# Kernel optimization log

Measured on AMD Instinct MI355X. Metric: run time of the kernel, lower is better.

Reference implementation:

```python
import jax, jax.numpy as jnp
import numpy as np

OUT, IN, GS = 8192, 8192, 128
N_GROUPS = OUT * IN // GS  # 524288


def setup_inputs() -> dict:
    key = jax.random.key(0)
    k1, k2, k3 = jax.random.split(key, 3)
    x = jax.random.normal(k1, (32, IN), dtype=jnp.float32)
    # ternary values in {-1, 0, 1}
    ternary = jax.random.randint(k2, (OUT, IN), -1, 2, dtype=jnp.int32)
    # positive per-group scales
    scales = jax.random.uniform(k3, (N_GROUPS,), dtype=jnp.float32, minval=0.01, maxval=0.1)
    return {"x": x, "ternary": ternary, "scales": scales}


def reference(x, ternary, scales):
    # Dequantize: each contiguous group of GS weights shares one scale.
    # scales: [n_groups] -> [n_groups, GS] -> [OUT, IN]
    scales_exp = jnp.broadcast_to(scales[:, None], (N_GROUPS, GS)).reshape(OUT, IN)
    w = ternary.astype(jnp.float32) * scales_exp  # [OUT, IN]
    # F.linear(x, w) = x @ w.T
    return jnp.einsum("ti,oi->to", x, w)
```

## Files before the change

kernel.cpp:

```cpp
#include <hip/hip_runtime.h>
#include <stdint.h>

#define OUT_DIM 8192
#define IN_DIM  8192
#define GS      128
#define MROWS   32
#define NSPLIT  8
#define KCHUNK  1024
#define KS      64
#define NSTG    (KCHUNK / KS)
#define PART_ELEMS (MROWS * OUT_DIM)

typedef __attribute__((ext_vector_type(8))) short bf16x8;
typedef __attribute__((ext_vector_type(4))) float f32x4;
typedef __attribute__((ext_vector_type(8))) unsigned short u16x8;
typedef __attribute__((ext_vector_type(2))) unsigned short u16x2;
typedef __attribute__((ext_vector_type(4))) unsigned int   u32x4;

__device__ __forceinline__ unsigned short f2bf_rne(float f) {
    uint32_t v = __builtin_bit_cast(uint32_t, f);
    v += 0x7FFFu + ((v >> 16) & 1u);
    return (unsigned short)(v >> 16);
}

__global__ __launch_bounds__(256) void prep_xbf(const float* __restrict__ x,
                                                unsigned short* __restrict__ xbf) {
    int i = (blockIdx.x * 256 + threadIdx.x) * 8;
    float4 a = *(const float4*)(x + i);
    float4 b = *(const float4*)(x + i + 4);
    float f[8] = {a.x, a.y, a.z, a.w, b.x, b.y, b.z, b.w};
    u16x8 u;
#pragma unroll
    for (int j = 0; j < 8; ++j) u[j] = f2bf_rne(f[j]);
    *(u16x8*)(xbf + i) = u;
}

__device__ __forceinline__ unsigned int cvt2(int t0, int t1, unsigned int p32) {
    unsigned int t16 = __builtin_amdgcn_perm((unsigned int)t1, (unsigned int)t0,
                                             0x05040100u);
    unsigned int v   = p32 | (t16 & 0x80008000u);
    u16x2 r = __builtin_bit_cast(u16x2, v) *
              __builtin_bit_cast(u16x2, t16 & 0x00010001u);
    return __builtin_bit_cast(unsigned int, r);
}

__device__ __forceinline__ bf16x8 conv8(const int4 wa, const int4 wb, unsigned int p32) {
    u32x4 d;
    d[0] = cvt2(wa.x, wa.y, p32);
    d[1] = cvt2(wa.z, wa.w, p32);
    d[2] = cvt2(wb.x, wb.y, p32);
    d[3] = cvt2(wb.z, wb.w, p32);
    return __builtin_bit_cast(bf16x8, d);
}

#define WSW(r, c) ((c) ^ (((r) & 7) << 3))
__global__ __launch_bounds__(256) void ternary_gemm(
    const int* __restrict__ tern, const float* __restrict__ scales,
    const unsigned short* __restrict__ xbf, float* __restrict__ part) {
    __shared__ __align__(16) int            lw[64][68];
    __shared__ __align__(16) unsigned short lx[32][72];

    const int tid  = threadIdx.x;
    const int wv   = tid >> 6;
    const int lane = tid & 63;
    const int n    = lane & 15;
    const int quad = lane >> 4;

    const int otile = blockIdx.x & 127;
    const int kc    = blockIdx.x >> 7;
    const int o0    = otile << 6;
    const int o     = o0 + (wv << 4) + n;
    const int kpos0 = kc << 10;

    const int srow = tid >> 4;
    const int scol = (tid & 15) << 2;
    const int* __restrict__ wbase = tern + (size_t)o0 * IN_DIM + kpos0 + scol;

    const int xrow = tid >> 3;
    const int xcol = (tid & 7) << 3;
    const unsigned short* __restrict__ xbase =
        xbf + (size_t)xrow * IN_DIM + kpos0 + xcol;

    const float* __restrict__ sp = scales + o * (IN_DIM / GS) + (kc << 3);

    f32x4 acc0 = {0.f, 0.f, 0.f, 0.f};
    f32x4 acc1 = {0.f, 0.f, 0.f, 0.f};

#define WLOAD(d0, d1, d2, d3, T) do { const int* wb = wbase + (T) * KS;        \
        d0 = *(const int4*)(wb + (size_t) srow       * IN_DIM);                \
        d1 = *(const int4*)(wb + (size_t)(srow + 16) * IN_DIM);                \
        d2 = *(const int4*)(wb + (size_t)(srow + 32) * IN_DIM);                \
        d3 = *(const int4*)(wb + (size_t)(srow + 48) * IN_DIM); } while (0)
#define XLOAD(d, T) (d) = *(const bf16x8*)(xbase + (T) * KS)
#define WWRITE(s0, s1, s2, s3) do { const int c = WSW(srow, scol);             \
        *(int4*)&lw[srow     ][c] = s0; *(int4*)&lw[srow + 16][c] = s1;        \
        *(int4*)&lw[srow + 32][c] = s2; *(int4*)&lw[srow + 48][c] = s3; } while (0)
#define XWRITE(v) *(bf16x8*)&lx[xrow][WSW(xrow, xcol)] = (v)

    int4 wn0, wn1, wn2, wn3; bf16x8 xn;
    WLOAD(wn0, wn1, wn2, wn3, 0); XLOAD(xn, 0);
    WWRITE(wn0, wn1, wn2, wn3);   XWRITE(xn);
    WLOAD(wn0, wn1, wn2, wn3, 1); XLOAD(xn, 1);
    int4 wf0 = wn0, wf1 = wn1, wf2 = wn2, wf3 = wn3; bf16x8 xf = xn;
    __syncthreads();

    const int lrow = (wv << 4) + n;
    const int qo   = quad << 3;

#pragma unroll 1
    for (int s = 0; s < NSTG; ++s) {
        if (s + 2 < NSTG) { WLOAD(wf0, wf1, wf2, wf3, s + 2); XLOAD(xf, s + 2); }
        const unsigned int ph  = f2bf_rne(sp[s >> 1]);
        const unsigned int p32 = ph | (ph << 16);
#pragma unroll
        for (int half = 0; half < 2; ++half) {
            const int kk  = (half << 5) + qo;
            const int wc  = WSW(lrow, kk);
            int4 w0 = *(const int4*)&lw[lrow][wc];
            int4 w1 = *(const int4*)&lw[lrow][wc + 4];
            bf16x8 a0 = *(const bf16x8*)&lx[n     ][WSW(n, kk)];
            bf16x8 a1 = *(const bf16x8*)&lx[16 + n][WSW(n, kk)];
            bf16x8 bfr = conv8(w0, w1, p32);
            acc0 = __builtin_amdgcn_mfma_f32_16x16x32_bf16(a0, bfr, acc0, 0, 0, 0);
            acc1 = __builtin_amdgcn_mfma_f32_16x16x32_bf16(a1, bfr, acc1, 0, 0, 0);
        }
        __syncthreads();
        if (s + 1 < NSTG) { WWRITE(wn0, wn1, wn2, wn3); XWRITE(xn); }
        __syncthreads();
        wn0 = wf0; wn1 = wf1; wn2 = wf2; wn3 = wf3; xn = xf;
    }
#undef WLOAD
#undef XLOAD
#undef WWRITE
#undef XWRITE

    float* __restrict__ prow = part + (size_t)kc * PART_ELEMS;
#pragma unroll
    for (int r = 0; r < 4; ++r) {
        prow[(quad * 4 + r) * OUT_DIM + o]      = acc0[r];
        prow[(quad * 4 + r + 16) * OUT_DIM + o] = acc1[r];
    }
}

__global__ __launch_bounds__(256) void reduce_parts(const float* __restrict__ part,
                                                    float* __restrict__ out) {
    const int i = (blockIdx.x * 256 + threadIdx.x) * 4;
    float4 s = *(const float4*)(part + i);
#pragma unroll
    for (int kc = 1; kc < NSPLIT; ++kc) {
        float4 v = *(const float4*)(part + (size_t)kc * PART_ELEMS + i);
        s.x += v.x; s.y += v.y; s.z += v.z; s.w += v.w;
    }
    *(float4*)(out + i) = s;
}

extern "C" void kernel_launch(void* const* d_in, const int* in_sizes, int n_in,
                              void* d_out, int out_size, void* d_ws, size_t ws_size,
                              hipStream_t stream) {
    const float* x      = (const float*)d_in[0];
    const int*   tern   = (const int*)d_in[1];
    const float* scales = (const float*)d_in[2];
    float* out = (float*)d_out;

    unsigned short* xbf = (unsigned short*)d_ws;
    float* part = (float*)((char*)d_ws + (512 << 10));

    prep_xbf<<<128, 256, 0, stream>>>(x, xbf);
    ternary_gemm<<<128 * NSPLIT, 256, 0, stream>>>(tern, scales, xbf, part);
    reduce_parts<<<256, 256, 0, stream>>>(part, out);
}
```

Before: 412.7 us.

## Stream ternary weights via direct global-to-LDS loads with double buffering

Replaces register-staged weight loads and manual LDS writes with global_load_lds direct-to-LDS copies into a double-buffered shared tile of 128-wide K stages, removing one barrier per stage. The x activations are now read directly from global memory (likely L2-cached) instead of being staged through LDS. This aims to cut VGPR pressure and LDS write instructions in the memory-bound weight stream, at the cost of unswizzled LDS reads (possible bank conflicts) and only one stage of prefetch depth.

```diff
diff --git a/kernel.cpp b/kernel.cpp
--- a/kernel.cpp
+++ b/kernel.cpp
@@ -7,8 +7,8 @@
 #define MROWS   32
 #define NSPLIT  8
 #define KCHUNK  1024
-#define KS      64
-#define NSTG    (KCHUNK / KS)
+#define KSTG    128
+#define NSTG    (KCHUNK / KSTG)
 #define PART_ELEMS (MROWS * OUT_DIM)
 
 typedef __attribute__((ext_vector_type(8))) short bf16x8;
@@ -53,12 +53,16 @@
     return __builtin_bit_cast(bf16x8, d);
 }
 
-#define WSW(r, c) ((c) ^ (((r) & 7) << 3))
+__device__ __forceinline__ void glds16(const int* g, int* l) {
+    __builtin_amdgcn_global_load_lds(
+        (const __attribute__((address_space(1))) void*)g,
+        (__attribute__((address_space(3))) void*)l, 16, 0, 0);
+}
+
 __global__ __launch_bounds__(256) void ternary_gemm(
     const int* __restrict__ tern, const float* __restrict__ scales,
     const unsigned short* __restrict__ xbf, float* __restrict__ part) {
-    __shared__ __align__(16) int            lw[64][68];
-    __shared__ __align__(16) unsigned short lx[32][72];
+    __shared__ __align__(16) int lw[2][64][KSTG];
 
     const int tid  = threadIdx.x;
     const int wv   = tid >> 6;
@@ -72,67 +76,51 @@
     const int o     = o0 + (wv << 4) + n;
     const int kpos0 = kc << 10;
 
-    const int srow = tid >> 4;
-    const int scol = (tid & 15) << 2;
-    const int* __restrict__ wbase = tern + (size_t)o0 * IN_DIM + kpos0 + scol;
+    const int rbase = (wv << 4);
+    const int* __restrict__ gstg =
+        tern + kpos0 + ((lane & 31) << 2) + (size_t)(o0 + rbase + (lane >> 5)) * IN_DIM;
 
-    const int xrow = tid >> 3;
-    const int xcol = (tid & 7) << 3;
-    const unsigned short* __restrict__ xbase =
-        xbf + (size_t)xrow * IN_DIM + kpos0 + xcol;
-
+    const unsigned short* __restrict__ xr0 = xbf + n * IN_DIM + kpos0 + (quad << 3);
+    const unsigned short* __restrict__ xr1 = xbf + (16 + n) * IN_DIM + kpos0 + (quad << 3);
     const float* __restrict__ sp = scales + o * (IN_DIM / GS) + (kc << 3);
 
     f32x4 acc0 = {0.f, 0.f, 0.f, 0.f};
     f32x4 acc1 = {0.f, 0.f, 0.f, 0.f};
 
-#define WLOAD(d0, d1, d2, d3, T) do { const int* wb = wbase + (T) * KS;        \
-        d0 = *(const int4*)(wb + (size_t) srow       * IN_DIM);                \
-        d1 = *(const int4*)(wb + (size_t)(srow + 16) * IN_DIM);                \
-        d2 = *(const int4*)(wb + (size_t)(srow + 32) * IN_DIM);                \
-        d3 = *(const int4*)(wb + (size_t)(srow + 48) * IN_DIM); } while (0)
-#define XLOAD(d, T) (d) = *(const bf16x8*)(xbase + (T) * KS)
-#define WWRITE(s0, s1, s2, s3) do { const int c = WSW(srow, scol);             \
-        *(int4*)&lw[srow     ][c] = s0; *(int4*)&lw[srow + 16][c] = s1;        \
-        *(int4*)&lw[srow + 32][c] = s2; *(int4*)&lw[srow + 48][c] = s3; } while (0)
-#define XWRITE(v) *(bf16x8*)&lx[xrow][WSW(xrow, xcol)] = (v)
+#define GLDS_STAGE(BUF, STG) do {                                              \
+        const int* gs = gstg + (STG) * KSTG;                                   \
+        _Pragma("unroll")                                                      \
+        for (int i = 0; i < 8; ++i)                                            \
+            glds16(gs + (size_t)(i << 1) * IN_DIM,                             \
+                   &lw[BUF][rbase + (i << 1)][0]);                             \
+    } while (0)
 
-    int4 wn0, wn1, wn2, wn3; bf16x8 xn;
-    WLOAD(wn0, wn1, wn2, wn3, 0); XLOAD(xn, 0);
-    WWRITE(wn0, wn1, wn2, wn3);   XWRITE(xn);
-    WLOAD(wn0, wn1, wn2, wn3, 1); XLOAD(xn, 1);
-    int4 wf0 = wn0, wf1 = wn1, wf2 = wn2, wf3 = wn3; bf16x8 xf = xn;
+    GLDS_STAGE(0, 0);
     __syncthreads();
 
     const int lrow = (wv << 4) + n;
-    const int qo   = quad << 3;
 
 #pragma unroll 1
     for (int s = 0; s < NSTG; ++s) {
-        if (s + 2 < NSTG) { WLOAD(wf0, wf1, wf2, wf3, s + 2); XLOAD(xf, s + 2); }
-        const unsigned int ph  = f2bf_rne(sp[s >> 1]);
+        const int buf = s & 1;
+        if (s + 1 < NSTG) GLDS_STAGE(buf ^ 1, s + 1);
+        const unsigned int ph  = f2bf_rne(sp[s]);
         const unsigned int p32 = ph | (ph << 16);
+        const int ks = s * KSTG;
 #pragma unroll
-        for (int half = 0; half < 2; ++half) {
-            const int kk  = (half << 5) + qo;
-            const int wc  = WSW(lrow, kk);
-            int4 w0 = *(const int4*)&lw[lrow][wc];
-            int4 w1 = *(const int4*)&lw[lrow][wc + 4];
-            bf16x8 a0 = *(const bf16x8*)&lx[n     ][WSW(n, kk)];
-            bf16x8 a1 = *(const bf16x8*)&lx[16 + n][WSW(n, kk)];
+        for (int half = 0; half < 4; ++half) {
+            const int koff = (half << 5) + (quad << 3);
+            int4 w0 = *(const int4*)&lw[buf][lrow][koff];
+            int4 w1 = *(const int4*)&lw[buf][lrow][koff + 4];
+            bf16x8 a0 = *(const bf16x8*)(xr0 + ks + (half << 5));
+            bf16x8 a1 = *(const bf16x8*)(xr1 + ks + (half << 5));
             bf16x8 bfr = conv8(w0, w1, p32);
             acc0 = __builtin_amdgcn_mfma_f32_16x16x32_bf16(a0, bfr, acc0, 0, 0, 0);
             acc1 = __builtin_amdgcn_mfma_f32_16x16x32_bf16(a1, bfr, acc1, 0, 0, 0);
         }
         __syncthreads();
-        if (s + 1 < NSTG) { WWRITE(wn0, wn1, wn2, wn3); XWRITE(xn); }
-        __syncthreads();
-        wn0 = wf0; wn1 = wf1; wn2 = wf2; wn3 = wf3; xn = xf;
     }
-#undef WLOAD
-#undef XLOAD
-#undef WWRITE
-#undef XWRITE
+#undef GLDS_STAGE
 
     float* __restrict__ prow = part + (size_t)kc * PART_ELEMS;
 #pragma unroll
```

Result: faster. 382.4 us (-7.3%).
